# Kernel optimization log

Hardware: AMD Instinct MI355X
Metric: run time of the kernel (lower is better)

Reference implementation:

```python
import jax, jax.numpy as jnp
import numpy as np

K = 3
KK = K * K
EPS = 1e-5


def conv2d(x, w, b, pad):
    y = jax.lax.conv_general_dilated(x, w, (1, 1), [(pad, pad), (pad, pad)],
                                     dimension_numbers=("NCHW", "OIHW", "NCHW"))
    return y + b[None, :, None, None]


def bn(x, g, b, m, v):
    inv = g / jnp.sqrt(v + EPS)
    return x * inv[None, :, None, None] + (b - m * inv)[None, :, None, None]


def deform_sample(x, dy, dx):
    # x: [B,C,H,W]; dy,dx: [B,KK,H,W] -> sampled [B,C,KK,H,W] (bilinear, zeros outside)
    B, C, H, W = x.shape
    k = jnp.arange(K, dtype=x.dtype) - 1.0  # pad=1, dilation=1, stride=1
    ky = jnp.repeat(k, K)  # [KK] row offsets
    kx = jnp.tile(k, K)    # [KK] col offsets
    hh = jnp.arange(H, dtype=x.dtype)
    ww = jnp.arange(W, dtype=x.dtype)
    py = hh[None, :, None] + ky[:, None, None] + dy  # [B,KK,H,W]
    px = ww[None, None, :] + kx[:, None, None] + dx

    def sample_one(img, py, px):
        y0f = jnp.floor(py); x0f = jnp.floor(px)
        wy = py - y0f; wx = px - x0f
        y0 = y0f.astype(jnp.int32); x0 = x0f.astype(jnp.int32)

        def gather(yi, xi, w):
            valid = (yi >= 0) & (yi < H) & (xi >= 0) & (xi < W)
            yc = jnp.clip(yi, 0, H - 1); xc = jnp.clip(xi, 0, W - 1)
            v = img[:, yc, xc]  # [C,KK,H,W]
            return v * (w * valid)[None]

        return (gather(y0, x0, (1 - wy) * (1 - wx)) +
                gather(y0, x0 + 1, (1 - wy) * wx) +
                gather(y0 + 1, x0, wy * (1 - wx)) +
                gather(y0 + 1, x0 + 1, wy * wx))

    return jax.vmap(sample_one)(x, py, px)


def setup_inputs() -> dict:
    key = jax.random.key(0)
    ks = jax.random.split(key, 16)
    B, C, H, W = 8, 256, 64, 64
    d = {
        "feature": jax.random.normal(ks[0], (B, C, H, W), jnp.float32),
        "p1_w": jax.random.normal(ks[1], (C, C, 1, 1), jnp.float32) * 0.05,
        "p1_b": jax.random.normal(ks[2], (C,), jnp.float32) * 0.05,
        "bn1_g": jax.random.normal(ks[3], (C,), jnp.float32) * 0.1 + 1.0,
        "bn1_b": jax.random.normal(ks[4], (C,), jnp.float32) * 0.05,
        "bn1_m": jax.random.normal(ks[5], (C,), jnp.float32) * 0.05,
        "bn1_v": jax.random.uniform(ks[6], (C,), jnp.float32) + 0.5,
        "off_w": jax.random.normal(ks[7], (3 * KK, 2 * C, K, K), jnp.float32) * 0.01,
        "off_b": jax.random.normal(ks[8], (3 * KK,), jnp.float32) * 0.01,
        "dcn_w": jax.random.normal(ks[9], (C, C, K, K), jnp.float32) * 0.05,
        "dcn_b": jax.random.normal(ks[10], (C,), jnp.float32) * 0.05,
        "bn2_g": jax.random.normal(ks[11], (C,), jnp.float32) * 0.1 + 1.0,
        "bn2_b": jax.random.normal(ks[12], (C,), jnp.float32) * 0.05,
        "bn2_m": jax.random.normal(ks[13], (C,), jnp.float32) * 0.05,
        "bn2_v": jax.random.uniform(ks[14], (C,), jnp.float32) + 0.5,
    }
    return d


def reference(feature, p1_w, p1_b, bn1_g, bn1_b, bn1_m, bn1_v,
              off_w, off_b, dcn_w, dcn_b, bn2_g, bn2_b, bn2_m, bn2_v):
    flipped = feature[..., ::-1]                      # flip last (W) axis
    proj = bn(conv2d(feature, p1_w, p1_b, 0), bn1_g, bn1_b, bn1_m, bn1_v)
    # DCNv2: offsets/mask from concat(flipped, proj)
    concat = jnp.concatenate([flipped, proj], axis=1)
    off = conv2d(concat, off_w, off_b, 1)             # [B,27,H,W]
    dy = off[:, :KK]
    dx = off[:, KK:2 * KK]
    mask = jax.nn.sigmoid(off[:, 2 * KK:])            # [B,KK,H,W]
    sampled = deform_sample(flipped, dy, dx)          # [B,C,KK,H,W]
    O = dcn_w.shape[0]
    y = jnp.einsum("bckhw,ock->bohw", sampled * mask[:, None], dcn_w.reshape(O, -1, KK))
    y = y + dcn_b[None, :, None, None]
    y = bn(y, bn2_g, bn2_b, bn2_m, bn2_v)
    return jax.nn.relu(proj + y)
```

## Files before the change

kernel.cpp:

```cpp
#include <hip/hip_runtime.h>
#include <hip/hip_bf16.h>
#include <math.h>

typedef __attribute__((ext_vector_type(8))) short short8;
typedef __attribute__((ext_vector_type(4))) short short4v;
typedef __attribute__((ext_vector_type(4))) float f32x4;
typedef __attribute__((ext_vector_type(2))) float f32x2;

__device__ __forceinline__ float bs2f(short s){
    union { unsigned u; float f; } x; x.u = ((unsigned)(unsigned short)s) << 16; return x.f;
}
__device__ __forceinline__ short f2bs(float f){
    union { float f; unsigned u; } x; x.f = f;
    unsigned r = x.u + 0x7fff + ((x.u >> 16) & 1);
    return (short)(r >> 16);
}
__device__ __forceinline__ f32x2 up2(unsigned u){
    union { unsigned u; float f; } lo, hi;
    lo.u = u << 16; hi.u = u & 0xffff0000u;
    f32x2 r; r.x = lo.f; r.y = hi.f; return r;
}
__device__ __forceinline__ unsigned pk2rn(float lo, float hi){
    __hip_bfloat162 h = __float22bfloat162_rn(make_float2(lo, hi));
    union { __hip_bfloat162 h; unsigned u; } cv; cv.h = h; return cv.u;
}
__device__ __forceinline__ void gl2lds16(const void* g, void* l){
    __builtin_amdgcn_global_load_lds(
        (const __attribute__((address_space(1))) void*)g,
        (__attribute__((address_space(3))) void*)l, 16, 0, 0);
}
__device__ __forceinline__ void hard_barrier(){
    __builtin_amdgcn_sched_barrier(0);
    __builtin_amdgcn_s_barrier();
    __builtin_amdgcn_sched_barrier(0);
}
__device__ __forceinline__ void lds_barrier(){
    __builtin_amdgcn_sched_barrier(0);
    asm volatile("s_waitcnt lgkmcnt(0)" ::: "memory");
    __builtin_amdgcn_s_barrier();
    __builtin_amdgcn_sched_barrier(0);
}

#define XPB ((size_t)66*66*512)


__global__ void k_prep(const float* __restrict__ p1_w, const float* __restrict__ p1_b,
                       const float* __restrict__ bn1_g, const float* __restrict__ bn1_b,
                       const float* __restrict__ bn1_m, const float* __restrict__ bn1_v,
                       const float* __restrict__ off_w,
                       const float* __restrict__ dcn_w, const float* __restrict__ dcn_b,
                       const float* __restrict__ bn2_g, const float* __restrict__ bn2_b,
                       const float* __restrict__ bn2_m, const float* __restrict__ bn2_v,
                       short* __restrict__ p1_wb, short* __restrict__ Woffb,
                       short* __restrict__ Wfrag,
                       float* __restrict__ bias1f, float* __restrict__ inv2f,
                       float* __restrict__ bias2f, unsigned* __restrict__ XpadU)
{
    int blk = blockIdx.x, t = threadIdx.x;
    if (blk == 0) {
        float inv1 = bn1_g[t] / sqrtf(bn1_v[t] + 1e-5f);
        bias1f[t] = p1_b[t] * inv1 + bn1_b[t] - bn1_m[t] * inv1;
        float inv2 = bn2_g[t] / sqrtf(bn2_v[t] + 1e-5f);
        inv2f[t] = inv2;
        bias2f[t] = dcn_b[t] * inv2 + bn2_b[t] - bn2_m[t] * inv2;
    } else if (blk <= 256) {
        int o = blk - 1;
        float inv1 = bn1_g[o] / sqrtf(bn1_v[o] + 1e-5f);
        p1_wb[o*256 + t] = f2bs(p1_w[o*256 + t] * inv1);
    } else if (blk <= 512) {
        int o = blk - 257;
        const float* src = dcn_w + (size_t)o*2304;
        uint4* dst = (uint4*)Wfrag;
        int strip = o >> 4, lnn = o & 15;
        #pragma unroll
        for (int r = 0; r < 2; ++r) {
            int j = r*256 + t;
            if (j < 288) {
                int tap = j >> 5, c0 = (j & 31) * 8;
                union { short s[8]; uint4 u; } v;
                #pragma unroll
                for (int e = 0; e < 8; ++e)
                    v.s[e] = f2bs(src[(c0 + e)*9 + tap]);
                dst[(size_t)((j >> 2)*16 + strip)*64 + (j & 3)*16 + lnn] = v.u;
            }
        }
    } else if (blk <= 544) {
        int oc = blk - 513;
        if (oc < 27) {
            const float* src = off_w + (size_t)oc*4608;
            #pragma unroll
            for (int j = 0; j < 18; ++j) {
                int e = j*256 + t, tap = e >> 9, ci = e & 511;
                Woffb[(size_t)oc*4608 + e] = f2bs(src[ci*9 + tap]);
            }
        } else {
            #pragma unroll
            for (int j = 0; j < 18; ++j)
                Woffb[(size_t)oc*4608 + j*256 + t] = 0;
        }
    } else {
        int hb = blk - 545;
        int b = hb / 260, i = hb % 260;
        int y, x;
        if (i < 66)       { y = 0;  x = i; }
        else if (i < 132) { y = 65; x = i - 66; }
        else { int j = i - 132; y = 1 + (j >> 1); x = (j & 1) * 65; }
        XpadU[((size_t)(b*66 + y)*66 + x)*256 + t] = 0u;
    }
}

__global__ void k_featT(const float* __restrict__ feature, short* __restrict__ Xpad)
{
    __shared__ float tile[64][65];
    int bb = blockIdx.x;
    int b = bb & 7, h = (bb >> 3) & 63, cg = bb >> 9;
    int c0 = cg * 64;
    int t = threadIdx.x;
    int lw = t & 63, li = t >> 6;
    #pragma unroll
    for (int j = 0; j < 16; ++j) {
        int cl = j*4 + li;
        tile[cl][63 - lw] = feature[((b*256 + c0 + cl)*64 + h)*64 + lw];
    }
    __syncthreads();
    #pragma unroll
    for (int j = 0; j < 16; ++j) {
        int wl = j*4 + li;
        Xpad[((size_t)(b*66 + h+1)*66 + (wl+1))*512 + c0 + lw] = f2bs(tile[lw][wl]);
    }
}

__global__ __launch_bounds__(512, 4) void k_projm(
    short* Xpad, const short* __restrict__ p1_wb, const float* __restrict__ bias1f)
{
    __shared__ short Ash[256*32];
    __shared__ short Bsh[64*32];
    int bid = blockIdx.x;
    int b = bid & 7, h = bid >> 3;
    int t = threadIdx.x;
    int lane = t & 63, w = t >> 6;
    int ln = lane & 15, q = lane >> 4;
    int r16 = lane >> 2;
    int sq  = (lane & 3) ^ ((lane >> 3) & 3);
    int rq  = (q ^ ((ln >> 1) & 3)) * 8;
    size_t rowbase = (size_t)(b*66 + h + 1)*66;

    f32x4 acc[2][4] = {};
    for (int kt = 0; kt < 8; ++kt) {
        int kcol = kt*32 + sq*8;
        #pragma unroll
        for (int i = 0; i < 2; ++i) {
            int row = w*32 + i*16 + r16;
            gl2lds16(p1_wb + (size_t)row*256 + kcol, Ash + (w*32 + i*16)*32);
        }
        if (w < 4) {
            int x = w*16 + r16;
            gl2lds16(Xpad + (rowbase + (64 - x))*512 + kcol, Bsh + (w*16)*32);
        }
        __syncthreads();
        short8 af[2], bfr[4];
        #pragma unroll
        for (int i = 0; i < 2; ++i)
            af[i] = *(const short8*)&Ash[(w*32 + i*16 + ln)*32 + rq];
        #pragma unroll
        for (int j = 0; j < 4; ++j)
            bfr[j] = *(const short8*)&Bsh[(j*16 + ln)*32 + rq];
        #pragma unroll
        for (int i = 0; i < 2; ++i)
            #pragma unroll
            for (int j = 0; j < 4; ++j)
                acc[i][j] = __builtin_amdgcn_mfma_f32_16x16x32_bf16(af[i], bfr[j], acc[i][j], 0, 0, 0);
        __syncthreads();
    }
    #pragma unroll
    for (int i = 0; i < 2; ++i) {
        int ob = w*32 + i*16 + q*4;
        #pragma unroll
        for (int j = 0; j < 4; ++j) {
            int x = j*16 + ln;
            size_t xb = (rowbase + x + 1)*512 + 256 + ob;
            short4v st;
            st.x = f2bs(acc[i][j][0] + bias1f[ob]);
            st.y = f2bs(acc[i][j][1] + bias1f[ob+1]);
            st.z = f2bs(acc[i][j][2] + bias1f[ob+2]);
            st.w = f2bs(acc[i][j][3] + bias1f[ob+3]);
            *(short4v*)&Xpad[xb] = st;
        }
    }
}

__global__ __launch_bounds__(512, 4) void k_offm(
    const short* __restrict__ Xpad, const short* __restrict__ Woffb,
    const float* __restrict__ off_b, float* __restrict__ offv)
{
    __shared__ short Ash[8][32*32];
    __shared__ short Bsh[8][64*32];
    int bid = blockIdx.x;
    int b = bid & 7, h = bid >> 3;
    int t = threadIdx.x;
    int lane = t & 63, w = t >> 6;
    int ln = lane & 15, q = lane >> 4;
    int wr = w >> 2, wc = w & 3;
    int r16 = lane >> 2;
    int sq  = (lane & 3) ^ ((lane >> 3) & 3);
    int rq  = (q ^ ((ln >> 1) & 3)) * 8;
    const short* xb = Xpad + (size_t)b*XPB;

    f32x4 acc = {};
    for (int it = 0; it < 18; ++it) {
        #pragma unroll
        for (int s = 0; s < 8; ++s) {
            int k = it*256 + s*32;
            int tap = k >> 9;
            int dy = tap/3 - 1, dx = tap%3 - 1;
            if (w < 4) {
                int row = w*16 + r16;
                const short* gB = xb + ((size_t)(h + 1 + dy)*66 + (row + dx + 1))*512
                                     + (k & 511) + sq*8;
                gl2lds16(gB, &Bsh[s][(w*16)*32]);
            } else if (w < 6) {
                int row = (w-4)*16 + r16;
                const short* gA = Woffb + (size_t)row*4608 + k + sq*8;
                gl2lds16(gA, &Ash[s][((w-4)*16)*32]);
            }
        }
        __syncthreads();
        #pragma unroll
        for (int s = 0; s < 8; ++s) {
            short8 af  = *(const short8*)&Ash[s][(wr*16 + ln)*32 + rq];
            short8 bfr = *(const short8*)&Bsh[s][(wc*16 + ln)*32 + rq];
            acc = __builtin_amdgcn_mfma_f32_16x16x32_bf16(af, bfr, acc, 0, 0, 0);
        }
        __syncthreads();
    }
    int x = wc*16 + ln;
    #pragma unroll
    for (int r = 0; r < 4; ++r) {
        int oc = wr*16 + q*4 + r;
        if (oc < 27)
            offv[((b*27 + oc)*64 + h)*64 + x] = acc[r] + off_b[oc];
    }
}

#define ALOAD4(kn_, A_)                                                   \
    A_##0 = Wf4[(size_t)(((kn_)*2+0)*16 + tw0)*64 + lane];                \
    A_##1 = Wf4[(size_t)(((kn_)*2+0)*16 + tw1)*64 + lane];                \
    A_##2 = Wf4[(size_t)(((kn_)*2+1)*16 + tw0)*64 + lane];                \
    A_##3 = Wf4[(size_t)(((kn_)*2+1)*16 + tw1)*64 + lane];

#define MMPHASE(A_)                                                       \
    {                                                                     \
        short8 af00 = *(short8*)&A_##0, af01 = *(short8*)&A_##1;          \
        short8 af10 = *(short8*)&A_##2, af11 = *(short8*)&A_##3;          \
        short8 bfr;                                                       \
        _Pragma("unroll")                                                 \
        for (int jj = 0; jj < 4; ++jj) {                                  \
            bfr = *(const short8*)&Bsh[0][(jj*16 + ln)*32 + rq];          \
            acc[0][jj] = __builtin_amdgcn_mfma_f32_16x16x32_bf16(af00, bfr, acc[0][jj], 0, 0, 0); \
            acc[1][jj] = __builtin_amdgcn_mfma_f32_16x16x32_bf16(af01, bfr, acc[1][jj], 0, 0, 0); \
        }                                                                 \
        _Pragma("unroll")                                                 \
        for (int jj = 0; jj < 4; ++jj) {                                  \
            bfr = *(const short8*)&Bsh[1][(jj*16 + ln)*32 + rq];          \
            acc[0][jj] = __builtin_amdgcn_mfma_f32_16x16x32_bf16(af10, bfr, acc[0][jj], 0, 0, 0); \
            acc[1][jj] = __builtin_amdgcn_mfma_f32_16x16x32_bf16(af11, bfr, acc[1][jj], 0, 0, 0); \
        }                                                                 \
    }

#define WINX(kc2_, AC_, AN_, UC_, VN_)                                    \
    {                                                                     \
        int kn_ = (kc2_) < 35 ? (kc2_) + 1 : 35;                          \
        ALOAD4(kn_, AN_);                                                 \
        GATHER(kn_, VN_);                                                 \
        __builtin_amdgcn_sched_barrier(0);                                \
        BLEND(UC_, (kc2_) >> 2);                                          \
        lds_barrier();                                                    \
        MMPHASE(AC_);                                                     \
        hard_barrier();                                                   \
    }

__global__ __launch_bounds__(512, 3) void k_gemm(
    const short* __restrict__ Xpad,
    const short* __restrict__ Wfrag,
    const float* __restrict__ offv,
    const float* __restrict__ inv2f, const float* __restrict__ bias2f,
    float* __restrict__ out)
{
    __shared__ __align__(16) short Bsh[2][64*32];
    __shared__ unsigned c_pk[576];
    __shared__ float c_w[576*4];
    int bid = blockIdx.x;
    int b = bid & 7, h = bid >> 3;
    int t = threadIdx.x;
    int lane = t & 63, w = t >> 6;
    int ln = lane & 15, q = lane >> 4;
    int rq  = (q ^ ((ln >> 1) & 3)) * 8;
    int tw0 = w*2, tw1 = w*2 + 1;
    const uint4* Wf4 = (const uint4*)Wfrag;

    for (int e = t; e < 576; e += 512) {
        int p = e / 9, k = e % 9;
        int base = (b*27)*4096 + h*64 + p;
        float dy = offv[base + k*4096];
        float dx = offv[base + (9+k)*4096];
        float ms = offv[base + (18+k)*4096];
        ms = 1.f / (1.f + expf(-ms));
        float py = (float)h + (float)(k/3 - 1) + dy;
        float px = (float)p + (float)(k%3 - 1) + dx;
        float y0f = floorf(py), x0f = floorf(px);
        float wy = py - y0f, wx = px - x0f;
        int y0 = (int)y0f, x0 = (int)x0f;
        int y1 = y0 + 1, x1 = x0 + 1;
        float vy0 = (y0 >= 0 && y0 < 64) ? 1.f : 0.f;
        float vy1 = (y1 >= 0 && y1 < 64) ? 1.f : 0.f;
        float vx0 = (x0 >= 0 && x0 < 64) ? 1.f : 0.f;
        float vx1 = (x1 >= 0 && x1 < 64) ? 1.f : 0.f;
        int y0c = min(max(y0,0),63), y1c = min(max(y1,0),63);
        int x0c = min(max(x0,0),63), x1c = min(max(x1,0),63);
        unsigned cell = (unsigned)(((y0c+1)*66 + x0c+1)*128);
        unsigned sx = (x1c != x0c) ? 1u : 0u;
        unsigned sy = (y1c != y0c) ? 1u : 0u;
        c_pk[e] = cell | (sx << 20) | (sy << 21);
        c_w[e*4+0] = ms * (1.f-wy)*(1.f-wx) * vy0*vx0;
        c_w[e*4+1] = ms * (1.f-wy)*wx       * vy0*vx1;
        c_w[e*4+2] = ms * wy*(1.f-wx)       * vy1*vx0;
        c_w[e*4+3] = ms * wy*wx             * vy1*vx1;
    }
    __syncthreads();

    const uint2* fT = (const uint2*)Xpad + (size_t)b*(XPB/4);
    int pr = t >> 3;
    int jo = t & 7;
    int pe9 = pr*9;
    short* bdst = &Bsh[jo >> 2][pr*32 + (((jo & 3) ^ ((pr >> 1) & 3)) << 3)];

    f32x4 acc[2][4] = {};
    uint4 U[4], V[4];
    uint4 a00, a01, a02, a03;
    uint4 a10, a11, a12, a13;

    auto GATHER = [&](int win, uint4 (&dst)[4]) {
        unsigned pw = c_pk[pe9 + (win >> 2)];
        int o00 = pw & 0xFFFFF;
        int dxs = (pw >> 13) & 128;
        int dys = ((pw >> 8) & 0x2000) | ((pw >> 13) & 0x100);
        int cin = ((win & 3) << 4) + jo*2;
        const uint2* p0 = fT + (o00 + cin);
        dst[0] = *(const uint4*)(p0);
        dst[1] = *(const uint4*)(p0 + dxs);
        dst[2] = *(const uint4*)(p0 + dys);
        dst[3] = *(const uint4*)(p0 + dys + dxs);
    };
    auto BLEND = [&](uint4 (&uc)[4], int tap) {
        const float4 cw = *(const float4*)&c_w[(pe9 + tap)*4];
        f32x2 Wx; Wx.x = cw.x; Wx.y = cw.x;
        f32x2 Wy; Wy.x = cw.y; Wy.y = cw.y;
        f32x2 Wz; Wz.x = cw.z; Wz.y = cw.z;
        f32x2 Ww; Ww.x = cw.w; Ww.y = cw.w;
        f32x2 G0 = Wx*up2(uc[0].x) + Wy*up2(uc[1].x) + Wz*up2(uc[2].x) + Ww*up2(uc[3].x);
        f32x2 G1 = Wx*up2(uc[0].y) + Wy*up2(uc[1].y) + Wz*up2(uc[2].y) + Ww*up2(uc[3].y);
        f32x2 G2 = Wx*up2(uc[0].z) + Wy*up2(uc[1].z) + Wz*up2(uc[2].z) + Ww*up2(uc[3].z);
        f32x2 G3 = Wx*up2(uc[0].w) + Wy*up2(uc[1].w) + Wz*up2(uc[2].w) + Ww*up2(uc[3].w);
        uint4 pkv;
        pkv.x = pk2rn(G0.x, G0.y);
        pkv.y = pk2rn(G1.x, G1.y);
        pkv.z = pk2rn(G2.x, G2.y);
        pkv.w = pk2rn(G3.x, G3.y);
        *(uint4*)bdst = pkv;
    };

    ALOAD4(0, a0);
    GATHER(0, U);
    __builtin_amdgcn_sched_barrier(0);
    #pragma unroll 1
    for (int kc2 = 0; kc2 < 36; kc2 += 2) {
        WINX(kc2,     a0, a1, U, V);
        WINX(kc2 + 1, a1, a0, V, U);
    }

    #pragma unroll
    for (int i = 0; i < 2; ++i) {
        int ob = w*32 + i*16 + q*4;
        #pragma unroll
        for (int jj = 0; jj < 4; ++jj) {
            int p = jj*16 + ln;
            size_t xb = ((size_t)(b*66 + h + 1)*66 + p + 1)*512 + 256 + ob;
            short4v prr = *(const short4v*)&Xpad[xb];
            #pragma unroll
            for (int r = 0; r < 4; ++r) {
                int o = ob + r;
                size_t idx = ((size_t)(b*256 + o))*4096 + h*64 + p;
                float rs = bs2f(((const short*)&prr)[r]);
                float v = rs + acc[i][jj][r]*inv2f[o] + bias2f[o];
                out[idx] = v < 0.f ? 0.f : v;
            }
        }
    }
}

extern "C" void kernel_launch(void* const* d_in, const int* in_sizes, int n_in,
                              void* d_out, int out_size, void* d_ws, size_t ws_size,
                              hipStream_t stream)
{
    const float* feature = (const float*)d_in[0];
    const float* p1_w  = (const float*)d_in[1];
    const float* p1_b  = (const float*)d_in[2];
    const float* bn1_g = (const float*)d_in[3];
    const float* bn1_b = (const float*)d_in[4];
    const float* bn1_m = (const float*)d_in[5];
    const float* bn1_v = (const float*)d_in[6];
    const float* off_w = (const float*)d_in[7];
    const float* off_b = (const float*)d_in[8];
    const float* dcn_w = (const float*)d_in[9];
    const float* dcn_b = (const float*)d_in[10];
    const float* bn2_g = (const float*)d_in[11];
    const float* bn2_b = (const float*)d_in[12];
    const float* bn2_m = (const float*)d_in[13];
    const float* bn2_v = (const float*)d_in[14];

    float* ws = (float*)d_ws;
    short* Xpad   = (short*)ws;
    float* offbuf = ws + 8921088;
    short* p1_wb  = (short*)(ws + 9805824);
    short* Woffb  = (short*)(ws + 9838592);
    short* Wfrag  = (short*)(ws + 9912320);
    float* bias1f = ws + 10207232;
    float* inv2f  = ws + 10207488;
    float* bias2f = ws + 10207744;

    k_prep<<<2625, 256, 0, stream>>>(p1_w, p1_b, bn1_g, bn1_b, bn1_m, bn1_v,
                                     off_w, dcn_w, dcn_b, bn2_g, bn2_b, bn2_m, bn2_v,
                                     p1_wb, Woffb, Wfrag, bias1f, inv2f, bias2f,
                                     (unsigned*)Xpad);
    k_featT<<<2048, 256, 0, stream>>>(feature, Xpad);
    k_projm<<<512, 512, 0, stream>>>(Xpad, p1_wb, bias1f);
    k_offm<<<512, 512, 0, stream>>>(Xpad, Woffb, off_b, offbuf);
    k_gemm<<<512, 512, 0, stream>>>(Xpad, Wfrag, offbuf, inv2f, bias2f, (float*)d_out);
}
```

Baseline: 220.1 us.

## Double-buffer LDS B tile and overlap MFMA with gather/blend, raise occupancy

Restructures the deformable GEMM main loop to use two LDS B buffers. The MFMA phase now reads the current buffer while the next window's gather, weight load and blend write into the other buffer, which cuts the loop from two barriers per step to one. It drops the register double-buffering of the A fragments and gathered values to free registers, raises launch_bounds min blocks from 3 to 4, and raises wave priority during the MFMA phase. The trade-off is twice the LDS for B tiles and less latency hiding for the A loads, which are now issued after the MFMAs.

```diff
diff --git a/kernel.cpp b/kernel.cpp
--- a/kernel.cpp
+++ b/kernel.cpp
@@ -242,51 +242,41 @@
     }
 }
 
-#define ALOAD4(kn_, A_)                                                   \
-    A_##0 = Wf4[(size_t)(((kn_)*2+0)*16 + tw0)*64 + lane];                \
-    A_##1 = Wf4[(size_t)(((kn_)*2+0)*16 + tw1)*64 + lane];                \
-    A_##2 = Wf4[(size_t)(((kn_)*2+1)*16 + tw0)*64 + lane];                \
-    A_##3 = Wf4[(size_t)(((kn_)*2+1)*16 + tw1)*64 + lane];
-
-#define MMPHASE(A_)                                                       \
+#define ALOAD4(kn_)                                                       \
+    a0 = Wf4[(size_t)(((kn_)*2+0)*16 + tw0)*64 + lane];                   \
+    a1 = Wf4[(size_t)(((kn_)*2+0)*16 + tw1)*64 + lane];                   \
+    a2 = Wf4[(size_t)(((kn_)*2+1)*16 + tw0)*64 + lane];                   \
+    a3 = Wf4[(size_t)(((kn_)*2+1)*16 + tw1)*64 + lane];
+
+#define MMPHASE(bufR_)                                                    \
     {                                                                     \
-        short8 af00 = *(short8*)&A_##0, af01 = *(short8*)&A_##1;          \
-        short8 af10 = *(short8*)&A_##2, af11 = *(short8*)&A_##3;          \
+        short8 af00 = *(short8*)&a0, af01 = *(short8*)&a1;                \
+        short8 af10 = *(short8*)&a2, af11 = *(short8*)&a3;                \
         short8 bfr;                                                       \
+        __builtin_amdgcn_s_setprio(1);                                    \
         _Pragma("unroll")                                                 \
         for (int jj = 0; jj < 4; ++jj) {                                  \
-            bfr = *(const short8*)&Bsh[0][(jj*16 + ln)*32 + rq];          \
+            bfr = *(const short8*)&(bufR_)[(jj*16 + ln)*32 + rq];         \
             acc[0][jj] = __builtin_amdgcn_mfma_f32_16x16x32_bf16(af00, bfr, acc[0][jj], 0, 0, 0); \
             acc[1][jj] = __builtin_amdgcn_mfma_f32_16x16x32_bf16(af01, bfr, acc[1][jj], 0, 0, 0); \
         }                                                                 \
         _Pragma("unroll")                                                 \
         for (int jj = 0; jj < 4; ++jj) {                                  \
-            bfr = *(const short8*)&Bsh[1][(jj*16 + ln)*32 + rq];          \
+            bfr = *(const short8*)&(bufR_)[2048 + (jj*16 + ln)*32 + rq];  \
             acc[0][jj] = __builtin_amdgcn_mfma_f32_16x16x32_bf16(af10, bfr, acc[0][jj], 0, 0, 0); \
             acc[1][jj] = __builtin_amdgcn_mfma_f32_16x16x32_bf16(af11, bfr, acc[1][jj], 0, 0, 0); \
         }                                                                 \
-    }
-
-#define WINX(kc2_, AC_, AN_, UC_, VN_)                                    \
-    {                                                                     \
-        int kn_ = (kc2_) < 35 ? (kc2_) + 1 : 35;                          \
-        ALOAD4(kn_, AN_);                                                 \
-        GATHER(kn_, VN_);                                                 \
-        __builtin_amdgcn_sched_barrier(0);                                \
-        BLEND(UC_, (kc2_) >> 2);                                          \
-        lds_barrier();                                                    \
-        MMPHASE(AC_);                                                     \
-        hard_barrier();                                                   \
-    }
-
-__global__ __launch_bounds__(512, 3) void k_gemm(
+        __builtin_amdgcn_s_setprio(0);                                    \
+    }
+
+__global__ __launch_bounds__(512, 4) void k_gemm(
     const short* __restrict__ Xpad,
     const short* __restrict__ Wfrag,
     const float* __restrict__ offv,
     const float* __restrict__ inv2f, const float* __restrict__ bias2f,
     float* __restrict__ out)
 {
-    __shared__ __align__(16) short Bsh[2][64*32];
+    __shared__ __align__(16) short Bsh[2][2][64*32];
     __shared__ unsigned c_pk[576];
     __shared__ float c_w[576*4];
     int bid = blockIdx.x;
@@ -332,50 +322,58 @@
     int pr = t >> 3;
     int jo = t & 7;
     int pe9 = pr*9;
-    short* bdst = &Bsh[jo >> 2][pr*32 + (((jo & 3) ^ ((pr >> 1) & 3)) << 3)];
+    int boff = (jo >> 2)*2048 + pr*32 + (((jo & 3) ^ ((pr >> 1) & 3)) << 3);
 
     f32x4 acc[2][4] = {};
-    uint4 U[4], V[4];
-    uint4 a00, a01, a02, a03;
-    uint4 a10, a11, a12, a13;
-
-    auto GATHER = [&](int win, uint4 (&dst)[4]) {
+    uint4 u[4];
+    uint4 a0, a1, a2, a3;
+
+    auto GATHER = [&](int win) {
         unsigned pw = c_pk[pe9 + (win >> 2)];
         int o00 = pw & 0xFFFFF;
         int dxs = (pw >> 13) & 128;
         int dys = ((pw >> 8) & 0x2000) | ((pw >> 13) & 0x100);
         int cin = ((win & 3) << 4) + jo*2;
         const uint2* p0 = fT + (o00 + cin);
-        dst[0] = *(const uint4*)(p0);
-        dst[1] = *(const uint4*)(p0 + dxs);
-        dst[2] = *(const uint4*)(p0 + dys);
-        dst[3] = *(const uint4*)(p0 + dys + dxs);
+        u[0] = *(const uint4*)(p0);
+        u[1] = *(const uint4*)(p0 + dxs);
+        u[2] = *(const uint4*)(p0 + dys);
+        u[3] = *(const uint4*)(p0 + dys + dxs);
     };
-    auto BLEND = [&](uint4 (&uc)[4], int tap) {
+    auto BLEND = [&](int tap, short* bufW) {
         const float4 cw = *(const float4*)&c_w[(pe9 + tap)*4];
         f32x2 Wx; Wx.x = cw.x; Wx.y = cw.x;
         f32x2 Wy; Wy.x = cw.y; Wy.y = cw.y;
         f32x2 Wz; Wz.x = cw.z; Wz.y = cw.z;
         f32x2 Ww; Ww.x = cw.w; Ww.y = cw.w;
-        f32x2 G0 = Wx*up2(uc[0].x) + Wy*up2(uc[1].x) + Wz*up2(uc[2].x) + Ww*up2(uc[3].x);
-        f32x2 G1 = Wx*up2(uc[0].y) + Wy*up2(uc[1].y) + Wz*up2(uc[2].y) + Ww*up2(uc[3].y);
-        f32x2 G2 = Wx*up2(uc[0].z) + Wy*up2(uc[1].z) + Wz*up2(uc[2].z) + Ww*up2(uc[3].z);
-        f32x2 G3 = Wx*up2(uc[0].w) + Wy*up2(uc[1].w) + Wz*up2(uc[2].w) + Ww*up2(uc[3].w);
+        f32x2 G0 = Wx*up2(u[0].x) + Wy*up2(u[1].x) + Wz*up2(u[2].x) + Ww*up2(u[3].x);
+        f32x2 G1 = Wx*up2(u[0].y) + Wy*up2(u[1].y) + Wz*up2(u[2].y) + Ww*up2(u[3].y);
+        f32x2 G2 = Wx*up2(u[0].z) + Wy*up2(u[1].z) + Wz*up2(u[2].z) + Ww*up2(u[3].z);
+        f32x2 G3 = Wx*up2(u[0].w) + Wy*up2(u[1].w) + Wz*up2(u[2].w) + Ww*up2(u[3].w);
         uint4 pkv;
         pkv.x = pk2rn(G0.x, G0.y);
         pkv.y = pk2rn(G1.x, G1.y);
         pkv.z = pk2rn(G2.x, G2.y);
         pkv.w = pk2rn(G3.x, G3.y);
-        *(uint4*)bdst = pkv;
+        *(uint4*)&bufW[boff] = pkv;
     };
 
-    ALOAD4(0, a0);
-    GATHER(0, U);
-    __builtin_amdgcn_sched_barrier(0);
-    #pragma unroll 1
-    for (int kc2 = 0; kc2 < 36; kc2 += 2) {
-        WINX(kc2,     a0, a1, U, V);
-        WINX(kc2 + 1, a1, a0, V, U);
+    GATHER(0);
+    BLEND(0, &Bsh[0][0][0]);
+    ALOAD4(0);
+    lds_barrier();
+
+    #pragma unroll 2
+    for (int kc2 = 0; kc2 < 36; ++kc2) {
+        int kn = kc2 < 35 ? kc2 + 1 : 35;
+        short* bufR = &Bsh[kc2 & 1][0][0];
+        short* bufW = &Bsh[(kc2 & 1) ^ 1][0][0];
+        GATHER(kn);
+        __builtin_amdgcn_sched_barrier(0);
+        MMPHASE(bufR);
+        ALOAD4(kn);
+        BLEND(kn >> 2, bufW);
+        lds_barrier();
     }
 
     #pragma unroll
```

Result: no change. 220.0 us (-0.1%).

## Fuse feature transpose into projection GEMM and pre-fragment offset-conv weights

Applied to the files above, without the earlier changes.

The transpose/flip/bf16 pack kernel is merged into the 1x1 projection GEMM. Each block now transposes its row of the feature map into LDS and builds the swizzled B operand there directly, so the projection no longer re-reads Xpad from global memory and one launch goes away. The offset-conv weights are pre-packed in k_prep into MFMA fragment order, so k_offm loads the A operand straight into registers instead of staging it through LDS. In exchange, k_fproj does more serial work per block, since one block handles all 256 channels, and it runs at lower occupancy (launch bounds 2) with more LDS per block.

```diff
diff --git a/kernel.cpp b/kernel.cpp
--- a/kernel.cpp
+++ b/kernel.cpp
@@ -51,7 +51,7 @@
                        const float* __restrict__ dcn_w, const float* __restrict__ dcn_b,
                        const float* __restrict__ bn2_g, const float* __restrict__ bn2_b,
                        const float* __restrict__ bn2_m, const float* __restrict__ bn2_v,
-                       short* __restrict__ p1_wb, short* __restrict__ Woffb,
+                       short* __restrict__ p1_wb, short* __restrict__ Wofrag,
                        short* __restrict__ Wfrag,
                        float* __restrict__ bias1f, float* __restrict__ inv2f,
                        float* __restrict__ bias2f, unsigned* __restrict__ XpadU)
@@ -84,22 +84,23 @@
                 dst[(size_t)((j >> 2)*16 + strip)*64 + (j & 3)*16 + lnn] = v.u;
             }
         }
-    } else if (blk <= 544) {
-        int oc = blk - 513;
-        if (oc < 27) {
-            const float* src = off_w + (size_t)oc*4608;
-            #pragma unroll
-            for (int j = 0; j < 18; ++j) {
-                int e = j*256 + t, tap = e >> 9, ci = e & 511;
-                Woffb[(size_t)oc*4608 + e] = f2bs(src[ci*9 + tap]);
-            }
-        } else {
-            #pragma unroll
-            for (int j = 0; j < 18; ++j)
-                Woffb[(size_t)oc*4608 + j*256 + t] = 0;
-        }
+    } else if (blk <= 584) {
+        int gidx = (blk - 513)*256 + t;
+        int kc = gidx >> 7;
+        int rem = gidx & 127;
+        int strip = rem >> 6, lane2 = rem & 63;
+        int ln2 = lane2 & 15, q2 = lane2 >> 4;
+        int row = strip*16 + ln2;
+        union { short s[8]; uint4 u; } v;
+        #pragma unroll
+        for (int e = 0; e < 8; ++e) {
+            int k = kc*32 + q2*8 + e;
+            int tap = k >> 9, ci = k & 511;
+            v.s[e] = (row < 27) ? f2bs(off_w[(size_t)row*4608 + ci*9 + tap]) : (short)0;
+        }
+        ((uint4*)Wofrag)[gidx] = v.u;
     } else {
-        int hb = blk - 545;
+        int hb = blk - 585;
         int b = hb / 260, i = hb % 260;
         int y, x;
         if (i < 66)       { y = 0;  x = i; }
@@ -109,42 +110,46 @@
     }
 }
 
-__global__ void k_featT(const float* __restrict__ feature, short* __restrict__ Xpad)
+__global__ __launch_bounds__(512, 2) void k_fproj(
+    const float* __restrict__ feature, short* Xpad,
+    const short* __restrict__ p1_wb, const float* __restrict__ bias1f)
 {
-    __shared__ float tile[64][65];
-    int bb = blockIdx.x;
-    int b = bb & 7, h = (bb >> 3) & 63, cg = bb >> 9;
-    int c0 = cg * 64;
-    int t = threadIdx.x;
-    int lw = t & 63, li = t >> 6;
-    #pragma unroll
-    for (int j = 0; j < 16; ++j) {
-        int cl = j*4 + li;
-        tile[cl][63 - lw] = feature[((b*256 + c0 + cl)*64 + h)*64 + lw];
-    }
-    __syncthreads();
-    #pragma unroll
-    for (int j = 0; j < 16; ++j) {
-        int wl = j*4 + li;
-        Xpad[((size_t)(b*66 + h+1)*66 + (wl+1))*512 + c0 + lw] = f2bs(tile[lw][wl]);
-    }
-}
-
-__global__ __launch_bounds__(512, 4) void k_projm(
-    short* Xpad, const short* __restrict__ p1_wb, const float* __restrict__ bias1f)
-{
-    __shared__ short Ash[256*32];
-    __shared__ short Bsh[64*32];
+    __shared__ __align__(16) unsigned char sh_u[16640];
+    __shared__ __align__(16) short Bt[8][2048];
+    float (*tile)[65] = (float(*)[65])sh_u;
+    short* Ash = (short*)sh_u;
     int bid = blockIdx.x;
     int b = bid & 7, h = bid >> 3;
     int t = threadIdx.x;
     int lane = t & 63, w = t >> 6;
+    int lw = t & 63, li = t >> 6;
     int ln = lane & 15, q = lane >> 4;
     int r16 = lane >> 2;
     int sq  = (lane & 3) ^ ((lane >> 3) & 3);
     int rq  = (q ^ ((ln >> 1) & 3)) * 8;
     size_t rowbase = (size_t)(b*66 + h + 1)*66;
 
+    for (int cg = 0; cg < 4; ++cg) {
+        int c0 = cg * 64;
+        #pragma unroll
+        for (int j = 0; j < 8; ++j) {
+            int cl = j*8 + li;
+            tile[cl][63 - lw] = feature[((b*256 + c0 + cl)*64 + h)*64 + lw];
+        }
+        __syncthreads();
+        #pragma unroll
+        for (int j = 0; j < 8; ++j) {
+            int x = j*8 + li;
+            short s  = f2bs(tile[lw][x]);
+            Xpad[(rowbase + x + 1)*512 + c0 + lw] = s;
+            short sB = f2bs(tile[lw][63 - x]);
+            int c = c0 + lw;
+            int kt = c >> 5, kk = c & 31, p = kk >> 3, e = kk & 7;
+            Bt[kt][x*32 + ((p ^ ((x >> 1) & 3)) << 3) + e] = sB;
+        }
+        __syncthreads();
+    }
+
     f32x4 acc[2][4] = {};
     for (int kt = 0; kt < 8; ++kt) {
         int kcol = kt*32 + sq*8;
@@ -153,10 +158,6 @@
             int row = w*32 + i*16 + r16;
             gl2lds16(p1_wb + (size_t)row*256 + kcol, Ash + (w*32 + i*16)*32);
         }
-        if (w < 4) {
-            int x = w*16 + r16;
-            gl2lds16(Xpad + (rowbase + (64 - x))*512 + kcol, Bsh + (w*16)*32);
-        }
         __syncthreads();
         short8 af[2], bfr[4];
         #pragma unroll
@@ -164,7 +165,7 @@
             af[i] = *(const short8*)&Ash[(w*32 + i*16 + ln)*32 + rq];
         #pragma unroll
         for (int j = 0; j < 4; ++j)
-            bfr[j] = *(const short8*)&Bsh[(j*16 + ln)*32 + rq];
+            bfr[j] = *(const short8*)&Bt[kt][(j*16 + ln)*32 + rq];
         #pragma unroll
         for (int i = 0; i < 2; ++i)
             #pragma unroll
@@ -190,10 +191,9 @@
 }
 
 __global__ __launch_bounds__(512, 4) void k_offm(
-    const short* __restrict__ Xpad, const short* __restrict__ Woffb,
+    const short* __restrict__ Xpad, const uint4* __restrict__ Wof4,
     const float* __restrict__ off_b, float* __restrict__ offv)
 {
-    __shared__ short Ash[8][32*32];
     __shared__ short Bsh[8][64*32];
     int bid = blockIdx.x;
     int b = bid & 7, h = bid >> 3;
@@ -208,26 +208,26 @@
 
     f32x4 acc = {};
     for (int it = 0; it < 18; ++it) {
-        #pragma unroll
-        for (int s = 0; s < 8; ++s) {
-            int k = it*256 + s*32;
-            int tap = k >> 9;
-            int dy = tap/3 - 1, dx = tap%3 - 1;
-            if (w < 4) {
-                int row = w*16 + r16;
+        int tap = it >> 1;
+        int dy = tap/3 - 1, dx = tap%3 - 1;
+        uint4 a[8];
+        #pragma unroll
+        for (int s = 0; s < 8; ++s)
+            a[s] = Wof4[(size_t)((it*8 + s)*2 + wr)*64 + lane];
+        {
+            int k = it*256 + w*32;
+            #pragma unroll
+            for (int g = 0; g < 4; ++g) {
+                int row = g*16 + r16;
                 const short* gB = xb + ((size_t)(h + 1 + dy)*66 + (row + dx + 1))*512
                                      + (k & 511) + sq*8;
-                gl2lds16(gB, &Bsh[s][(w*16)*32]);
-            } else if (w < 6) {
-                int row = (w-4)*16 + r16;
-                const short* gA = Woffb + (size_t)row*4608 + k + sq*8;
-                gl2lds16(gA, &Ash[s][((w-4)*16)*32]);
+                gl2lds16(gB, &Bsh[w][(g*16)*32]);
             }
         }
         __syncthreads();
         #pragma unroll
         for (int s = 0; s < 8; ++s) {
-            short8 af  = *(const short8*)&Ash[s][(wr*16 + ln)*32 + rq];
+            short8 af  = *(short8*)&a[s];
             short8 bfr = *(const short8*)&Bsh[s][(wc*16 + ln)*32 + rq];
             acc = __builtin_amdgcn_mfma_f32_16x16x32_bf16(af, bfr, acc, 0, 0, 0);
         }
@@ -422,18 +422,17 @@
     short* Xpad   = (short*)ws;
     float* offbuf = ws + 8921088;
     short* p1_wb  = (short*)(ws + 9805824);
-    short* Woffb  = (short*)(ws + 9838592);
+    short* Wofrag = (short*)(ws + 9838592);
     short* Wfrag  = (short*)(ws + 9912320);
     float* bias1f = ws + 10207232;
     float* inv2f  = ws + 10207488;
     float* bias2f = ws + 10207744;
 
-    k_prep<<<2625, 256, 0, stream>>>(p1_w, p1_b, bn1_g, bn1_b, bn1_m, bn1_v,
+    k_prep<<<2665, 256, 0, stream>>>(p1_w, p1_b, bn1_g, bn1_b, bn1_m, bn1_v,
                                      off_w, dcn_w, dcn_b, bn2_g, bn2_b, bn2_m, bn2_v,
-                                     p1_wb, Woffb, Wfrag, bias1f, inv2f, bias2f,
+                                     p1_wb, Wofrag, Wfrag, bias1f, inv2f, bias2f,
                                      (unsigned*)Xpad);
-    k_featT<<<2048, 256, 0, stream>>>(feature, Xpad);
-    k_projm<<<512, 512, 0, stream>>>(Xpad, p1_wb, bias1f);
-    k_offm<<<512, 512, 0, stream>>>(Xpad, Woffb, off_b, offbuf);
+    k_fproj<<<512, 512, 0, stream>>>(feature, Xpad, p1_wb, bias1f);
+    k_offm<<<512, 512, 0, stream>>>(Xpad, (const uint4*)Wofrag, off_b, offbuf);
     k_gemm<<<512, 512, 0, stream>>>(Xpad, Wfrag, offbuf, inv2f, bias2f, (float*)d_out);
 }
```

Result: no change. 222.6 us (+1.1%).
